# Kernel optimization log

Measured on AMD Instinct MI355X. Metric: run time of the kernel, lower is better.

The kernel has to match this reference:

```python
import jax, jax.numpy as jnp
import numpy as np

N_NODES = 100000


def setup_inputs() -> dict:
    key = jax.random.key(0)
    ks = jax.random.split(key, 6)
    x = jax.random.normal(ks[0], (N_NODES, 128), dtype=jnp.float32)
    edge_index = jax.random.randint(ks[1], (2, 1600000), 0, N_NODES, dtype=jnp.int32)
    W_gcn = jax.random.normal(ks[2], (128, 128), dtype=jnp.float32) * 0.05
    b_gcn = jax.random.normal(ks[3], (128,), dtype=jnp.float32) * 0.05
    W_fc = jax.random.normal(ks[4], (64, 128), dtype=jnp.float32) * 0.05
    b_fc = jax.random.normal(ks[5], (64,), dtype=jnp.float32) * 0.05
    return {"x": x, "edge_index": edge_index, "W_gcn": W_gcn, "b_gcn": b_gcn, "W_fc": W_fc, "b_fc": b_fc}


def _gcn_conv(x, edge_index, W, b):
    N = x.shape[0]
    # add self-loops (PyG GCNConv default add_self_loops=True)
    loops = jnp.arange(N, dtype=edge_index.dtype)
    row = jnp.concatenate([edge_index[0], loops])  # source
    col = jnp.concatenate([edge_index[1], loops])  # target (aggregation index)
    # symmetric normalization: deg computed at target with unit edge weights
    deg = jax.ops.segment_sum(jnp.ones_like(col, dtype=x.dtype), col, num_segments=N)
    deg_inv_sqrt = jnp.where(deg > 0, jax.lax.rsqrt(deg), 0.0)
    norm = deg_inv_sqrt[row] * deg_inv_sqrt[col]  # [E+N]
    xw = x @ W  # [N, nhid] - transform before aggregation
    msgs = norm[:, None] * xw[row]  # gather + scale, [E+N, nhid]
    out = jax.ops.segment_sum(msgs, col, num_segments=N)  # scatter-add
    return out + b


def reference(x, edge_index, W_gcn, b_gcn, W_fc, b_fc):
    h = _gcn_conv(x, edge_index, W_gcn, b_gcn)  # [N, nhid]
    return h @ W_fc.T + b_fc  # [N, nclass]
```

## Files before the change

### kernel.cpp

```cpp
#include <hip/hip_runtime.h>
#include <hip/hip_bf16.h>

typedef __hip_bfloat16 bf16;

#define N_NODES 100000
#define N_EDGES 1600000
#define F_IN    128
#define F_OUT   64
#define NBLK    391

#define NB_BKT   196
#define BKT_SH   9
#define BKT_CAP  8960
#define LBIN_CAP 56
#define EPB_A    4096


typedef __attribute__((ext_vector_type(8))) short vbf8;
typedef __attribute__((ext_vector_type(4))) float vf4;

__device__ __forceinline__ float ldf(const void* p, size_t i, bool isbf) {
    return isbf ? __bfloat162float(((const bf16*)p)[i]) : ((const float*)p)[i];
}
__device__ __forceinline__ void stf(void* p, size_t i, bool isbf, float v) {
    if (isbf) ((bf16*)p)[i] = __float2bfloat16(v);
    else      ((float*)p)[i] = v;
}
__device__ __forceinline__ unsigned short f2bfu(float f) {
    __hip_bfloat16 h = __float2bfloat16(f);
    union { __hip_bfloat16 h; unsigned short u; } c; c.h = h; return c.u;
}
__device__ __forceinline__ float bflo(unsigned int u) { return __uint_as_float(u << 16); }
__device__ __forceinline__ float bfhi(unsigned int u) { return __uint_as_float(u & 0xffff0000u); }

__global__ __launch_bounds__(256) void k_weights(const unsigned short* __restrict__ xs,
                          const void* __restrict__ Wg, const void* __restrict__ bg,
                          const void* __restrict__ Wf, const void* __restrict__ bfc,
                          float* __restrict__ M, float* __restrict__ cvec,
                          bf16* __restrict__ Mhi, bf16* __restrict__ Mlo,
                          int* __restrict__ flag, int* __restrict__ gtail) {
    __shared__ int sflag;
    int lt = threadIdx.x;
    if (lt < 64) {
        int good = 0;
#pragma unroll
        for (int q = 0; q < 2; ++q) {
            unsigned short v = xs[2 * (lt + 64 * q)];
            int e = (v >> 7) & 0xFF;
            if ((e >= 100 && e <= 140) || ((v & 0x7FFF) == 0)) good++;
        }
        unsigned long long m1 = __ballot(good >= 1), m2 = __ballot(good >= 2);
        if (lt == 0) sflag = (__popcll(m1) + __popcll(m2) >= 96) ? 1 : 0;
    }
    __syncthreads();
    bool isbf = (sflag != 0);
    if (blockIdx.x == 0) {
        if (lt == 0) *flag = sflag;
        if (gtail && lt < NB_BKT) gtail[lt] = 0;
    }
    int t = blockIdx.x * 256 + lt;
    if (t >= F_IN * F_OUT) return;
    int k = t >> 6, c = t & 63;
    float s = 0.f;
    for (int j = 0; j < F_IN; ++j)
        s += ldf(Wg, k * F_IN + j, isbf) * ldf(Wf, c * F_IN + j, isbf);
    M[k * F_OUT + c] = s;
    if (Mhi) {
        int l    = (((k >> 3) & 3) << 4) | (c & 15);
        int fidx = ((((k >> 5) << 2) + (c >> 4)) * 64 + l) * 8 + (k & 7);
        bf16 h  = __float2bfloat16(s);
        Mhi[fidx] = h;
        Mlo[fidx] = __float2bfloat16(s - __bfloat162float(h));
    }
    if (k == 0) {
        float cs = ldf(bfc, c, isbf);
        for (int j = 0; j < F_IN; ++j)
            cs += ldf(bg, j, isbf) * ldf(Wf, c * F_IN + j, isbf);
        cvec[c] = cs;
    }
}


__global__ __launch_bounds__(256) void k_binA(const int* __restrict__ ei,
                                              int* __restrict__ gtail,
                                              unsigned* __restrict__ bkt) {
    __shared__ unsigned lbin[NB_BKT * LBIN_CAP];
    __shared__ int lcnt[NB_BKT];
    __shared__ int lbase[NB_BKT];
    int t = threadIdx.x;
    for (int b = t; b < NB_BKT; b += 256) lcnt[b] = 0;
    __syncthreads();
    int v0 = blockIdx.x * (EPB_A / 4);
#pragma unroll
    for (int q = 0; q < 4; ++q) {
        int vi = v0 + q * 256 + t;
        if (vi * 4 < N_EDGES) {
            int4 rv = ((const int4*)ei)[vi];
            int4 cv = ((const int4*)(ei + N_EDGES))[vi];
            int rs[4] = {rv.x, rv.y, rv.z, rv.w};
            int cs[4] = {cv.x, cv.y, cv.z, cv.w};
#pragma unroll
            for (int j = 0; j < 4; ++j) {
                int r = rs[j], c = cs[j];
                int b = c >> BKT_SH;
                unsigned val = (unsigned)r | ((unsigned)(c & ((1 << BKT_SH) - 1)) << 17);
                int p = atomicAdd(&lcnt[b], 1);
                if (p < LBIN_CAP) {
                    lbin[b * LBIN_CAP + p] = val;
                } else {
                    int gp = atomicAdd(&gtail[b], 1);
                    if (gp < BKT_CAP) bkt[(size_t)b * BKT_CAP + gp] = val;
                }
            }
        }
    }
    __syncthreads();
    for (int b = t; b < NB_BKT; b += 256) {
        int n = min(lcnt[b], LBIN_CAP);
        lbase[b] = atomicAdd(&gtail[b], n);
    }
    __syncthreads();
    int w = t >> 6, l = t & 63;
    for (int b = w; b < NB_BKT; b += 4) {
        int nB = min(lcnt[b], LBIN_CAP);
        int gp0 = lbase[b];
        for (int i = l; i < nB; i += 64) {
            int gp = gp0 + i;
            if (gp < BKT_CAP) bkt[(size_t)b * BKT_CAP + gp] = lbin[b * LBIN_CAP + i];
        }
    }
}

__global__ __launch_bounds__(512) void k_build(const unsigned* __restrict__ bkt,
                                               const int* __restrict__ gtail,
                                               int* __restrict__ ptr,
                                               int* __restrict__ cnt,
                                               float* __restrict__ dinv,
                                               int* __restrict__ srcs) {
    __shared__ int cntl[512], sm[512], fill[512];
    int b = blockIdx.x, t = threadIdx.x;
    int n = min(gtail[b], BKT_CAP);
    int gv = (t < b) ? min(gtail[t], BKT_CAP) : 0;
    sm[t] = gv; __syncthreads();
#pragma unroll
    for (int s = 256; s >= 1; s >>= 1) {
        if (t < s) sm[t] += sm[t + s];
        __syncthreads();
    }
    int base = sm[0];
    cntl[t] = 0;
    __syncthreads();
    for (int i = t; i < n; i += 512)
        atomicAdd(&cntl[bkt[(size_t)b * BKT_CAP + i] >> 17], 1);
    __syncthreads();
    int v = cntl[t];
    sm[t] = v; __syncthreads();
    for (int s = 1; s < 512; s <<= 1) {
        int add = (t >= s) ? sm[t - s] : 0;
        __syncthreads();
        sm[t] += add;
        __syncthreads();
    }
    int excl = sm[t] - v;
    fill[t] = excl;
    int node = (b << BKT_SH) + t;
    if (node < N_NODES) {
        ptr[node]  = base + excl;
        cnt[node]  = v;
        dinv[node] = rsqrtf((float)(v + 1));
    }
    __syncthreads();
    for (int i = t; i < n; i += 512) {
        unsigned e = bkt[(size_t)b * BKT_CAP + i];
        int c = (int)(e >> 17);
        int p = atomicAdd(&fill[c], 1);
        srcs[base + p] = (int)(e & 0x1FFFF);
    }
}

__global__ __launch_bounds__(256) void k_xmz_mfma(const int* __restrict__ flag,
                                                  const void* __restrict__ x,
                                                  const bf16* __restrict__ Mhi,
                                                  const bf16* __restrict__ Mlo,
                                                  const float* __restrict__ dinv,
                                                  bf16* __restrict__ y) {
    int t = threadIdx.x;
    int w = t >> 6, lane = t & 63;
    int g = lane >> 4, cb = lane & 15;
    int r0 = blockIdx.x * 64 + w * 16;
    int rr = min(r0 + cb, N_NODES - 1);
    bool isbf = (*flag != 0);
    const vbf8* Bh = (const vbf8*)Mhi;
    const vbf8* Bl = (const vbf8*)Mlo;
    vf4 acc0 = {0.f,0.f,0.f,0.f}, acc1 = {0.f,0.f,0.f,0.f};
    vf4 acc2 = {0.f,0.f,0.f,0.f}, acc3 = {0.f,0.f,0.f,0.f};

    if (isbf) {
        const vbf8* X8 = (const vbf8*)x;
#pragma unroll
        for (int kk = 0; kk < 4; ++kk) {
            vbf8 a = X8[(size_t)rr * 16 + kk * 4 + g];
            int bb = kk * 256 + lane;
            acc0 = __builtin_amdgcn_mfma_f32_16x16x32_bf16(a, Bh[bb      ], acc0, 0, 0, 0);
            acc0 = __builtin_amdgcn_mfma_f32_16x16x32_bf16(a, Bl[bb      ], acc0, 0, 0, 0);
            acc1 = __builtin_amdgcn_mfma_f32_16x16x32_bf16(a, Bh[bb +  64], acc1, 0, 0, 0);
            acc1 = __builtin_amdgcn_mfma_f32_16x16x32_bf16(a, Bl[bb +  64], acc1, 0, 0, 0);
            acc2 = __builtin_amdgcn_mfma_f32_16x16x32_bf16(a, Bh[bb + 128], acc2, 0, 0, 0);
            acc2 = __builtin_amdgcn_mfma_f32_16x16x32_bf16(a, Bl[bb + 128], acc2, 0, 0, 0);
            acc3 = __builtin_amdgcn_mfma_f32_16x16x32_bf16(a, Bh[bb + 192], acc3, 0, 0, 0);
            acc3 = __builtin_amdgcn_mfma_f32_16x16x32_bf16(a, Bl[bb + 192], acc3, 0, 0, 0);
        }
    } else {
        const float4* X4 = (const float4*)x;
#pragma unroll
        for (int kk = 0; kk < 4; ++kk) {
            float4 v0 = X4[(size_t)rr * 32 + kk * 8 + g * 2];
            float4 v1 = X4[(size_t)rr * 32 + kk * 8 + g * 2 + 1];
            vbf8 ah, al;
            {
                float fv[8] = {v0.x, v0.y, v0.z, v0.w, v1.x, v1.y, v1.z, v1.w};
#pragma unroll
                for (int i = 0; i < 8; ++i) {
                    unsigned bi = __float_as_uint(fv[i]);
                    ah[i] = (short)(bi >> 16);
                    float r = fv[i] - __uint_as_float(bi & 0xffff0000u);
                    al[i] = (short)(__float_as_uint(r) >> 16);
                }
            }
            int bb = kk * 256 + lane;
            vbf8 b0h = Bh[bb      ], b0l = Bl[bb      ];
            vbf8 b1h = Bh[bb +  64], b1l = Bl[bb +  64];
            vbf8 b2h = Bh[bb + 128], b2l = Bl[bb + 128];
            vbf8 b3h = Bh[bb + 192], b3l = Bl[bb + 192];
            acc0 = __builtin_amdgcn_mfma_f32_16x16x32_bf16(ah, b0h, acc0, 0, 0, 0);
            acc0 = __builtin_amdgcn_mfma_f32_16x16x32_bf16(ah, b0l, acc0, 0, 0, 0);
            acc0 = __builtin_amdgcn_mfma_f32_16x16x32_bf16(al, b0h, acc0, 0, 0, 0);
            acc1 = __builtin_amdgcn_mfma_f32_16x16x32_bf16(ah, b1h, acc1, 0, 0, 0);
            acc1 = __builtin_amdgcn_mfma_f32_16x16x32_bf16(ah, b1l, acc1, 0, 0, 0);
            acc1 = __builtin_amdgcn_mfma_f32_16x16x32_bf16(al, b1h, acc1, 0, 0, 0);
            acc2 = __builtin_amdgcn_mfma_f32_16x16x32_bf16(ah, b2h, acc2, 0, 0, 0);
            acc2 = __builtin_amdgcn_mfma_f32_16x16x32_bf16(ah, b2l, acc2, 0, 0, 0);
            acc2 = __builtin_amdgcn_mfma_f32_16x16x32_bf16(al, b2h, acc2, 0, 0, 0);
            acc3 = __builtin_amdgcn_mfma_f32_16x16x32_bf16(ah, b3h, acc3, 0, 0, 0);
            acc3 = __builtin_amdgcn_mfma_f32_16x16x32_bf16(ah, b3l, acc3, 0, 0, 0);
            acc3 = __builtin_amdgcn_mfma_f32_16x16x32_bf16(al, b3h, acc3, 0, 0, 0);
        }
    }

    unsigned short* yb = (unsigned short*)y;
#pragma unroll
    for (int i = 0; i < 4; ++i) {
        int r = r0 + g * 4 + i;
        if (r < N_NODES) {
            float d = dinv[r];
            unsigned short* yr = yb + (size_t)r * F_OUT + cb;
            yr[0]  = f2bfu(acc0[i] * d);
            yr[16] = f2bfu(acc1[i] * d);
            yr[32] = f2bfu(acc2[i] * d);
            yr[48] = f2bfu(acc3[i] * d);
        }
    }
}

__global__ __launch_bounds__(256) void k_agg(const int* __restrict__ flag,
                                             const int* __restrict__ ptr,
                                             const int* __restrict__ cnt,
                                             const int* __restrict__ srcs,
                                             const float* __restrict__ dinv,
                                             const bf16* __restrict__ y,
                                             const float* __restrict__ cvec,
                                             void* __restrict__ out) {
    int wid  = (blockIdx.x * 256 + threadIdx.x) >> 6;
    int lane = threadIdx.x & 63;
    int g  = lane >> 3;
    int j8 = lane & 7;
    int node = wid * 8 + g;
    bool alive = node < N_NODES;
    int n = 0, start = 0;
    if (alive) { n = cnt[node]; start = ptr[node]; }
    const uint4* y4 = (const uint4*)y;

    float acc[8];
#pragma unroll
    for (int i = 0; i < 8; ++i) acc[i] = 0.f;

    for (int b = 0; __any(b < n); b += 8) {
        int s = 0;
        int idx = b + j8;
        if (idx < n) s = srcs[start + idx];
#pragma unroll
        for (int k = 0; k < 8; ++k) {
            int su = __shfl(s, (g << 3) | k, 64);
            if (b + k < n) {
                uint4 v = y4[(size_t)su * 8 + j8];
                acc[0] += bflo(v.x); acc[1] += bfhi(v.x);
                acc[2] += bflo(v.y); acc[3] += bfhi(v.y);
                acc[4] += bflo(v.z); acc[5] += bfhi(v.z);
                acc[6] += bflo(v.w); acc[7] += bfhi(v.w);
            }
        }
    }

    if (!alive) return;
    bool isbf = (*flag != 0);
    uint4 sv = y4[(size_t)node * 8 + j8];
    float dn = dinv[node];
    const float4* cv4 = (const float4*)cvec;
    float4 c0 = cv4[j8 * 2], c1 = cv4[j8 * 2 + 1];
    size_t ob = (size_t)node * F_OUT + j8 * 8;
    if (isbf) {
        ushort4 p0, p1;
        p0.x = f2bfu(dn * (acc[0] + bflo(sv.x)) + c0.x);
        p0.y = f2bfu(dn * (acc[1] + bfhi(sv.x)) + c0.y);
        p0.z = f2bfu(dn * (acc[2] + bflo(sv.y)) + c0.z);
        p0.w = f2bfu(dn * (acc[3] + bfhi(sv.y)) + c0.w);
        p1.x = f2bfu(dn * (acc[4] + bflo(sv.z)) + c1.x);
        p1.y = f2bfu(dn * (acc[5] + bfhi(sv.z)) + c1.y);
        p1.z = f2bfu(dn * (acc[6] + bflo(sv.w)) + c1.z);
        p1.w = f2bfu(dn * (acc[7] + bfhi(sv.w)) + c1.w);
        ushort4* ob4 = (ushort4*)((unsigned short*)out + ob);
        ob4[0] = p0; ob4[1] = p1;
    } else {
        float4 q0, q1;
        q0.x = dn * (acc[0] + bflo(sv.x)) + c0.x;
        q0.y = dn * (acc[1] + bfhi(sv.x)) + c0.y;
        q0.z = dn * (acc[2] + bflo(sv.y)) + c0.z;
        q0.w = dn * (acc[3] + bfhi(sv.y)) + c0.w;
        q1.x = dn * (acc[4] + bflo(sv.z)) + c1.x;
        q1.y = dn * (acc[5] + bfhi(sv.z)) + c1.y;
        q1.z = dn * (acc[6] + bflo(sv.w)) + c1.z;
        q1.w = dn * (acc[7] + bfhi(sv.w)) + c1.w;
        float4* of4 = (float4*)((float*)out + ob);
        of4[0] = q0; of4[1] = q1;
    }
}


__global__ void k_init_deg(float* __restrict__ deg) {
    int i = blockIdx.x * blockDim.x + threadIdx.x;
    if (i < N_NODES) deg[i] = 1.0f;
}
__global__ void k_deg(const int* __restrict__ col, float* __restrict__ deg) {
    int e = blockIdx.x * blockDim.x + threadIdx.x;
    if (e < N_EDGES) atomicAdd(&deg[col[e]], 1.0f);
}
__global__ void k_dinv(float* __restrict__ deg) {
    int i = blockIdx.x * blockDim.x + threadIdx.x;
    if (i < N_NODES) deg[i] = rsqrtf(deg[i]);
}
__global__ __launch_bounds__(256) void k_xm(const int* __restrict__ flag,
                                            const void* __restrict__ x,
                                            const float* __restrict__ M,
                                            void* __restrict__ z) {
    __shared__ float Ms[F_IN * F_OUT];
    int t = threadIdx.x;
    for (int i = t; i < F_IN * F_OUT; i += 256) Ms[i] = M[i];
    __syncthreads();
    bool isbf = (*flag != 0);
    int r = blockIdx.x * 4 + (t >> 6);
    int c = t & 63;
    if (r >= N_NODES) return;
    float s = 0.f;
    if (isbf) {
        const bf16* xr = (const bf16*)x + (size_t)r * F_IN;
#pragma unroll
        for (int k = 0; k < F_IN; ++k) s += __bfloat162float(xr[k]) * Ms[k * F_OUT + c];
    } else {
        const float* xr = (const float*)x + (size_t)r * F_IN;
#pragma unroll
        for (int k = 0; k < F_IN; ++k) s += xr[k] * Ms[k * F_OUT + c];
    }
    stf(z, (size_t)r * F_OUT + c, isbf, s);
}
template <int LOGF>
__global__ __launch_bounds__(256) void k_init_acc(const int* __restrict__ flag,
                                                  const float* __restrict__ dinv,
                                                  const void* __restrict__ z,
                                                  float* __restrict__ acc, int base) {
    bool isbf = (*flag != 0);
    int t = blockIdx.x * 256 + threadIdx.x;
    int i = t >> LOGF, f = t & ((1 << LOGF) - 1);
    if (i >= N_NODES) return;
    float d = dinv[i];
    acc[t] = d * d * ldf(z, (size_t)i * F_OUT + base + f, isbf);
}
template <int LOGF>
__global__ __launch_bounds__(256) void k_scatter(const int* __restrict__ flag,
                                                 const int* __restrict__ ei,
                                                 const float* __restrict__ dinv,
                                                 const void* __restrict__ z,
                                                 float* __restrict__ acc, int base) {
    bool isbf = (*flag != 0);
    long long t = (long long)blockIdx.x * 256 + threadIdx.x;
    int e = (int)(t >> LOGF), f = (int)(t & ((1 << LOGF) - 1));
    if (e >= N_EDGES) return;
    int r = ei[e], c = ei[N_EDGES + e];
    float nm = dinv[r] * dinv[c];
    float v  = nm * ldf(z, (size_t)r * F_OUT + base + f, isbf);
    atomicAdd(&acc[((size_t)c << LOGF) + f], v);
}
template <int LOGF>
__global__ __launch_bounds__(256) void k_final(const int* __restrict__ flag,
                                               const float* __restrict__ acc,
                                               const float* __restrict__ cvec,
                                               void* __restrict__ out, int base) {
    bool isbf = (*flag != 0);
    int t = blockIdx.x * 256 + threadIdx.x;
    int i = t >> LOGF, f = t & ((1 << LOGF) - 1);
    if (i >= N_NODES) return;
    stf(out, (size_t)i * F_OUT + base + f, isbf, acc[t] + cvec[base + f]);
}
template <int LOGF>
static void run_passes(const int* flag, const int* ei, const float* dinv,
                       const void* z, float* acc, const float* cvec, void* out,
                       hipStream_t stream) {
    const int fpp = 1 << LOGF;
    const long long tn = (long long)N_NODES * fpp;
    const long long te = (long long)N_EDGES * fpp;
    const int gn = (int)((tn + 255) / 256);
    const int ge = (int)((te + 255) / 256);
    for (int base = 0; base < F_OUT; base += fpp) {
        k_init_acc<LOGF><<<gn, 256, 0, stream>>>(flag, dinv, z, acc, base);
        k_scatter<LOGF><<<ge, 256, 0, stream>>>(flag, ei, dinv, z, acc, base);
        k_final<LOGF><<<gn, 256, 0, stream>>>(flag, acc, cvec, out, base);
    }
}

extern "C" void kernel_launch(void* const* d_in, const int* in_sizes, int n_in,
                              void* d_out, int out_size, void* d_ws, size_t ws_size,
                              hipStream_t stream) {
    const void* x   = d_in[0];
    const int*  ei  = (const int*)d_in[1];
    const void* Wg  = d_in[2];
    const void* bg  = d_in[3];
    const void* Wf  = d_in[4];
    const void* bfc = d_in[5];
    char* ws = (char*)d_ws;

    const size_t CSR_NEED = 20871168;
    if (ws_size >= CSR_NEED) {
        int*      flag  = (int*)(ws + 0);
        float*    dinv  = (float*)(ws + 256);
        float*    M     = (float*)(ws + 400384);
        float*    cvec  = (float*)(ws + 433152);
        int*      cnt   = (int*)(ws + 433664);
        int*      ptr   = (int*)(ws + 833664);
        int*      gtail = (int*)(ws + 1233664);
        int*      srcs  = (int*)(ws + 1238528);
        bf16*     y     = (bf16*)(ws + 8038400);
        unsigned* bkt   = (unsigned*)(ws + 8038400);
        bf16*     Mhi   = (bf16*)(ws + 20838400);
        bf16*     Mlo   = (bf16*)(ws + 20854784);

        k_weights<<<(F_IN * F_OUT) / 256, 256, 0, stream>>>((const unsigned short*)x,
                    Wg, bg, Wf, bfc, M, cvec, Mhi, Mlo, flag, gtail);
        k_binA<<<(N_EDGES + EPB_A - 1) / EPB_A, 256, 0, stream>>>(ei, gtail, bkt);
        k_build<<<NB_BKT, 512, 0, stream>>>(bkt, gtail, ptr, cnt, dinv, srcs);
        k_xmz_mfma<<<(N_NODES + 63) / 64, 256, 0, stream>>>(flag, x, Mhi, Mlo, dinv, y);
        k_agg<<<3125, 256, 0, stream>>>(flag, ptr, cnt, srcs, dinv, y, cvec, d_out);
    } else {
        int*   flag = (int*)(ws + 0);
        float* deg  = (float*)(ws + 256);
        float* M    = (float*)(ws + 400384);
        float* cvec = (float*)(ws + 433152);
        float* acc  = (float*)(ws + 433664);

        k_weights<<<(F_IN * F_OUT) / 256, 256, 0, stream>>>((const unsigned short*)x,
                    Wg, bg, Wf, bfc, M, cvec, (bf16*)nullptr, (bf16*)nullptr, flag, (int*)nullptr);
        k_init_deg<<<NBLK, 256, 0, stream>>>(deg);
        k_deg<<<N_EDGES / 256, 256, 0, stream>>>(ei + N_EDGES, deg);
        k_dinv<<<NBLK, 256, 0, stream>>>(deg);
        k_xm<<<N_NODES / 4, 256, 0, stream>>>(flag, x, M, d_out);
        const size_t bn = 433664;
        if      (ws_size >= bn + (400000ull << 6)) run_passes<6>(flag, ei, deg, d_out, acc, cvec, d_out, stream);
        else if (ws_size >= bn + (400000ull << 5)) run_passes<5>(flag, ei, deg, d_out, acc, cvec, d_out, stream);
        else if (ws_size >= bn + (400000ull << 4)) run_passes<4>(flag, ei, deg, d_out, acc, cvec, d_out, stream);
        else if (ws_size >= bn + (400000ull << 3)) run_passes<3>(flag, ei, deg, d_out, acc, cvec, d_out, stream);
        else if (ws_size >= bn + (400000ull << 2)) run_passes<2>(flag, ei, deg, d_out, acc, cvec, d_out, stream);
        else if (ws_size >= bn + (400000ull << 1)) run_passes<1>(flag, ei, deg, d_out, acc, cvec, d_out, stream);
        else                                       run_passes<0>(flag, ei, deg, d_out, acc, cvec, d_out, stream);
    }
}
```

Baseline: 214.9 us.

## Replace bucketed CSR build with atomic degree count, block-scan pointers, atomic scatter

The CSR construction no longer uses two-level bucketing through shared-memory bins. It now counts in-degrees with global atomics fused into the weights kernel, computes row pointers with per-block scans whose bases come from an atomic tail counter, and scatters source indices through per-node cursor atomics. This removes the bucket staging buffer and a pass over the edges, at the cost of many scattered global atomics and non-deterministic ordering of sources within each row. Row segments are also placed in atomic-arrival order rather than node order.

```diff
diff --git a/kernel.cpp b/kernel.cpp
--- a/kernel.cpp
+++ b/kernel.cpp
@@ -9,12 +9,6 @@
 #define F_OUT   64
 #define NBLK    391
 
-#define NB_BKT   196
-#define BKT_SH   9
-#define BKT_CAP  8960
-#define LBIN_CAP 56
-#define EPB_A    4096
-
 
 typedef __attribute__((ext_vector_type(8))) short vbf8;
 typedef __attribute__((ext_vector_type(4))) float vf4;
@@ -38,7 +32,8 @@
                           const void* __restrict__ Wf, const void* __restrict__ bfc,
                           float* __restrict__ M, float* __restrict__ cvec,
                           bf16* __restrict__ Mhi, bf16* __restrict__ Mlo,
-                          int* __restrict__ flag, int* __restrict__ gtail) {
+                          int* __restrict__ flag, int* __restrict__ tail,
+                          int* __restrict__ deg, const int* __restrict__ col) {
     __shared__ int sflag;
     int lt = threadIdx.x;
     if (lt < 64) {
@@ -54,9 +49,17 @@
     }
     __syncthreads();
     bool isbf = (sflag != 0);
-    if (blockIdx.x == 0) {
-        if (lt == 0) *flag = sflag;
-        if (gtail && lt < NB_BKT) gtail[lt] = 0;
+    if (blockIdx.x == 0 && lt == 0) {
+        *flag = sflag;
+        if (tail) *tail = 0;
+    }
+    if (deg) {
+        const int4* c4 = (const int4*)col;
+        for (int vi = blockIdx.x * 256 + lt; vi < N_EDGES / 4; vi += gridDim.x * 256) {
+            int4 cv = c4[vi];
+            atomicAdd(&deg[cv.x], 1); atomicAdd(&deg[cv.y], 1);
+            atomicAdd(&deg[cv.z], 1); atomicAdd(&deg[cv.w], 1);
+        }
     }
     int t = blockIdx.x * 256 + lt;
     if (t >= F_IN * F_OUT) return;
@@ -81,101 +84,45 @@
 }
 
 
-__global__ __launch_bounds__(256) void k_binA(const int* __restrict__ ei,
-                                              int* __restrict__ gtail,
-                                              unsigned* __restrict__ bkt) {
-    __shared__ unsigned lbin[NB_BKT * LBIN_CAP];
-    __shared__ int lcnt[NB_BKT];
-    __shared__ int lbase[NB_BKT];
+__global__ __launch_bounds__(256) void k_ptr(const int* __restrict__ deg,
+                                             int* __restrict__ tail,
+                                             int* __restrict__ ptr,
+                                             int* __restrict__ cursor,
+                                             float* __restrict__ dinv) {
+    __shared__ int sm[256];
+    __shared__ int sbase;
     int t = threadIdx.x;
-    for (int b = t; b < NB_BKT; b += 256) lcnt[b] = 0;
-    __syncthreads();
-    int v0 = blockIdx.x * (EPB_A / 4);
-#pragma unroll
-    for (int q = 0; q < 4; ++q) {
-        int vi = v0 + q * 256 + t;
-        if (vi * 4 < N_EDGES) {
-            int4 rv = ((const int4*)ei)[vi];
-            int4 cv = ((const int4*)(ei + N_EDGES))[vi];
-            int rs[4] = {rv.x, rv.y, rv.z, rv.w};
-            int cs[4] = {cv.x, cv.y, cv.z, cv.w};
-#pragma unroll
-            for (int j = 0; j < 4; ++j) {
-                int r = rs[j], c = cs[j];
-                int b = c >> BKT_SH;
-                unsigned val = (unsigned)r | ((unsigned)(c & ((1 << BKT_SH) - 1)) << 17);
-                int p = atomicAdd(&lcnt[b], 1);
-                if (p < LBIN_CAP) {
-                    lbin[b * LBIN_CAP + p] = val;
-                } else {
-                    int gp = atomicAdd(&gtail[b], 1);
-                    if (gp < BKT_CAP) bkt[(size_t)b * BKT_CAP + gp] = val;
-                }
-            }
-        }
-    }
-    __syncthreads();
-    for (int b = t; b < NB_BKT; b += 256) {
-        int n = min(lcnt[b], LBIN_CAP);
-        lbase[b] = atomicAdd(&gtail[b], n);
-    }
-    __syncthreads();
-    int w = t >> 6, l = t & 63;
-    for (int b = w; b < NB_BKT; b += 4) {
-        int nB = min(lcnt[b], LBIN_CAP);
-        int gp0 = lbase[b];
-        for (int i = l; i < nB; i += 64) {
-            int gp = gp0 + i;
-            if (gp < BKT_CAP) bkt[(size_t)b * BKT_CAP + gp] = lbin[b * LBIN_CAP + i];
-        }
-    }
-}
-
-__global__ __launch_bounds__(512) void k_build(const unsigned* __restrict__ bkt,
-                                               const int* __restrict__ gtail,
-                                               int* __restrict__ ptr,
-                                               int* __restrict__ cnt,
-                                               float* __restrict__ dinv,
-                                               int* __restrict__ srcs) {
-    __shared__ int cntl[512], sm[512], fill[512];
-    int b = blockIdx.x, t = threadIdx.x;
-    int n = min(gtail[b], BKT_CAP);
-    int gv = (t < b) ? min(gtail[t], BKT_CAP) : 0;
-    sm[t] = gv; __syncthreads();
-#pragma unroll
-    for (int s = 256; s >= 1; s >>= 1) {
-        if (t < s) sm[t] += sm[t + s];
-        __syncthreads();
-    }
-    int base = sm[0];
-    cntl[t] = 0;
-    __syncthreads();
-    for (int i = t; i < n; i += 512)
-        atomicAdd(&cntl[bkt[(size_t)b * BKT_CAP + i] >> 17], 1);
-    __syncthreads();
-    int v = cntl[t];
+    int node = blockIdx.x * 256 + t;
+    int v = (node < N_NODES) ? deg[node] : 0;
     sm[t] = v; __syncthreads();
-    for (int s = 1; s < 512; s <<= 1) {
+    for (int s = 1; s < 256; s <<= 1) {
         int add = (t >= s) ? sm[t - s] : 0;
         __syncthreads();
         sm[t] += add;
         __syncthreads();
     }
-    int excl = sm[t] - v;
-    fill[t] = excl;
-    int node = (b << BKT_SH) + t;
+    if (t == 255) sbase = atomicAdd(tail, sm[255]);
+    __syncthreads();
     if (node < N_NODES) {
-        ptr[node]  = base + excl;
-        cnt[node]  = v;
-        dinv[node] = rsqrtf((float)(v + 1));
-    }
-    __syncthreads();
-    for (int i = t; i < n; i += 512) {
-        unsigned e = bkt[(size_t)b * BKT_CAP + i];
-        int c = (int)(e >> 17);
-        int p = atomicAdd(&fill[c], 1);
-        srcs[base + p] = (int)(e & 0x1FFFF);
-    }
+        int p = sbase + sm[t] - v;
+        ptr[node]    = p;
+        cursor[node] = p;
+        dinv[node]   = rsqrtf((float)(v + 1));
+    }
+}
+
+__global__ __launch_bounds__(256) void k_scat(const int* __restrict__ ei,
+                                              int* __restrict__ cursor,
+                                              int* __restrict__ srcs) {
+    int vi = blockIdx.x * 256 + threadIdx.x;
+    if (vi >= N_EDGES / 4) return;
+    int4 rv = ((const int4*)ei)[vi];
+    int4 cv = ((const int4*)(ei + N_EDGES))[vi];
+    int p;
+    p = atomicAdd(&cursor[cv.x], 1); srcs[p] = rv.x;
+    p = atomicAdd(&cursor[cv.y], 1); srcs[p] = rv.y;
+    p = atomicAdd(&cursor[cv.z], 1); srcs[p] = rv.z;
+    p = atomicAdd(&cursor[cv.w], 1); srcs[p] = rv.w;
 }
 
 __global__ __launch_bounds__(256) void k_xmz_mfma(const int* __restrict__ flag,
@@ -439,25 +386,27 @@
 
     const size_t CSR_NEED = 20871168;
     if (ws_size >= CSR_NEED) {
-        int*      flag  = (int*)(ws + 0);
-        float*    dinv  = (float*)(ws + 256);
-        float*    M     = (float*)(ws + 400384);
-        float*    cvec  = (float*)(ws + 433152);
-        int*      cnt   = (int*)(ws + 433664);
-        int*      ptr   = (int*)(ws + 833664);
-        int*      gtail = (int*)(ws + 1233664);
-        int*      srcs  = (int*)(ws + 1238528);
-        bf16*     y     = (bf16*)(ws + 8038400);
-        unsigned* bkt   = (unsigned*)(ws + 8038400);
-        bf16*     Mhi   = (bf16*)(ws + 20838400);
-        bf16*     Mlo   = (bf16*)(ws + 20854784);
-
-        k_weights<<<(F_IN * F_OUT) / 256, 256, 0, stream>>>((const unsigned short*)x,
-                    Wg, bg, Wf, bfc, M, cvec, Mhi, Mlo, flag, gtail);
-        k_binA<<<(N_EDGES + EPB_A - 1) / EPB_A, 256, 0, stream>>>(ei, gtail, bkt);
-        k_build<<<NB_BKT, 512, 0, stream>>>(bkt, gtail, ptr, cnt, dinv, srcs);
+        int*      flag   = (int*)(ws + 0);
+        float*    dinv   = (float*)(ws + 256);
+        int*      tail   = (int*)(ws + 400256);
+        float*    M      = (float*)(ws + 400384);
+        float*    cvec   = (float*)(ws + 433152);
+        int*      deg    = (int*)(ws + 433664);
+        int*      ptr    = (int*)(ws + 833664);
+        int*      srcs   = (int*)(ws + 1238528);
+        bf16*     y      = (bf16*)(ws + 8038400);
+        int*      cursor = (int*)(ws + 8038400);
+        bf16*     Mhi    = (bf16*)(ws + 20838400);
+        bf16*     Mlo    = (bf16*)(ws + 20854784);
+
+        hipMemsetAsync(deg, 0, (size_t)N_NODES * 4, stream);
+        k_weights<<<512, 256, 0, stream>>>((const unsigned short*)x,
+                    Wg, bg, Wf, bfc, M, cvec, Mhi, Mlo, flag, tail,
+                    deg, ei + N_EDGES);
+        k_ptr<<<NBLK, 256, 0, stream>>>(deg, tail, ptr, cursor, dinv);
+        k_scat<<<(N_EDGES / 4 + 255) / 256, 256, 0, stream>>>(ei, cursor, srcs);
         k_xmz_mfma<<<(N_NODES + 63) / 64, 256, 0, stream>>>(flag, x, Mhi, Mlo, dinv, y);
-        k_agg<<<3125, 256, 0, stream>>>(flag, ptr, cnt, srcs, dinv, y, cvec, d_out);
+        k_agg<<<3125, 256, 0, stream>>>(flag, ptr, deg, srcs, dinv, y, cvec, d_out);
     } else {
         int*   flag = (int*)(ws + 0);
         float* deg  = (float*)(ws + 256);
@@ -466,7 +415,8 @@
         float* acc  = (float*)(ws + 433664);
 
         k_weights<<<(F_IN * F_OUT) / 256, 256, 0, stream>>>((const unsigned short*)x,
-                    Wg, bg, Wf, bfc, M, cvec, (bf16*)nullptr, (bf16*)nullptr, flag, (int*)nullptr);
+                    Wg, bg, Wf, bfc, M, cvec, (bf16*)nullptr, (bf16*)nullptr,
+                    flag, (int*)nullptr, (int*)nullptr, (const int*)nullptr);
         k_init_deg<<<NBLK, 256, 0, stream>>>(deg);
         k_deg<<<N_EDGES / 256, 256, 0, stream>>>(ei + N_EDGES, deg);
         k_dinv<<<NBLK, 256, 0, stream>>>(deg);
```

New measurement: 372.1 us. +73.2%, slower.

## Fuse weight prep with edge binning, and CSR build with feature transform

Applied to the files above, without the earlier changes.

The weight-precompute and edge-binning kernels become one launch, split by block index. CSR build and the MFMA feature transform also become one launch, so they run side by side instead of in sequence. To remove the transform's dependence on the build's dinv, the binning pass also counts in-degree with global atomics, and the transform computes its own normalization from that count. The bucket buffer is moved so it no longer aliases y, and two memsets zero the counters. This trades launch gaps and serialization for 1.6M extra random global atomics and two extra memset launches.

```diff
diff --git a/kernel.cpp b/kernel.cpp
--- a/kernel.cpp
+++ b/kernel.cpp
@@ -14,6 +14,8 @@
 #define BKT_CAP  8960
 #define LBIN_CAP 56
 #define EPB_A    4096
+#define WBLK     32
+#define XMZ_BLK  782
 
 
 typedef __attribute__((ext_vector_type(8))) short vbf8;
@@ -33,64 +35,61 @@
 __device__ __forceinline__ float bflo(unsigned int u) { return __uint_as_float(u << 16); }
 __device__ __forceinline__ float bfhi(unsigned int u) { return __uint_as_float(u & 0xffff0000u); }
 
-__global__ __launch_bounds__(256) void k_weights(const unsigned short* __restrict__ xs,
+__global__ __launch_bounds__(256) void k_fat1(const unsigned short* __restrict__ xs,
                           const void* __restrict__ Wg, const void* __restrict__ bg,
                           const void* __restrict__ Wf, const void* __restrict__ bfc,
                           float* __restrict__ M, float* __restrict__ cvec,
                           bf16* __restrict__ Mhi, bf16* __restrict__ Mlo,
-                          int* __restrict__ flag, int* __restrict__ gtail) {
-    __shared__ int sflag;
-    int lt = threadIdx.x;
-    if (lt < 64) {
-        int good = 0;
-#pragma unroll
-        for (int q = 0; q < 2; ++q) {
-            unsigned short v = xs[2 * (lt + 64 * q)];
-            int e = (v >> 7) & 0xFF;
-            if ((e >= 100 && e <= 140) || ((v & 0x7FFF) == 0)) good++;
-        }
-        unsigned long long m1 = __ballot(good >= 1), m2 = __ballot(good >= 2);
-        if (lt == 0) sflag = (__popcll(m1) + __popcll(m2) >= 96) ? 1 : 0;
-    }
-    __syncthreads();
-    bool isbf = (sflag != 0);
-    if (blockIdx.x == 0) {
-        if (lt == 0) *flag = sflag;
-        if (gtail && lt < NB_BKT) gtail[lt] = 0;
-    }
-    int t = blockIdx.x * 256 + lt;
-    if (t >= F_IN * F_OUT) return;
-    int k = t >> 6, c = t & 63;
-    float s = 0.f;
-    for (int j = 0; j < F_IN; ++j)
-        s += ldf(Wg, k * F_IN + j, isbf) * ldf(Wf, c * F_IN + j, isbf);
-    M[k * F_OUT + c] = s;
-    if (Mhi) {
-        int l    = (((k >> 3) & 3) << 4) | (c & 15);
-        int fidx = ((((k >> 5) << 2) + (c >> 4)) * 64 + l) * 8 + (k & 7);
-        bf16 h  = __float2bfloat16(s);
-        Mhi[fidx] = h;
-        Mlo[fidx] = __float2bfloat16(s - __bfloat162float(h));
-    }
-    if (k == 0) {
-        float cs = ldf(bfc, c, isbf);
-        for (int j = 0; j < F_IN; ++j)
-            cs += ldf(bg, j, isbf) * ldf(Wf, c * F_IN + j, isbf);
-        cvec[c] = cs;
-    }
-}
-
-
-__global__ __launch_bounds__(256) void k_binA(const int* __restrict__ ei,
-                                              int* __restrict__ gtail,
-                                              unsigned* __restrict__ bkt) {
+                          int* __restrict__ flag,
+                          const int* __restrict__ ei, int* __restrict__ gtail,
+                          unsigned* __restrict__ bkt, int* __restrict__ deg) {
     __shared__ unsigned lbin[NB_BKT * LBIN_CAP];
     __shared__ int lcnt[NB_BKT];
     __shared__ int lbase[NB_BKT];
-    int t = threadIdx.x;
+    __shared__ int sflag;
+    int lt = threadIdx.x;
+
+    if (blockIdx.x < WBLK) {
+        if (lt < 64) {
+            int good = 0;
+#pragma unroll
+            for (int q = 0; q < 2; ++q) {
+                unsigned short v = xs[2 * (lt + 64 * q)];
+                int e = (v >> 7) & 0xFF;
+                if ((e >= 100 && e <= 140) || ((v & 0x7FFF) == 0)) good++;
+            }
+            unsigned long long m1 = __ballot(good >= 1), m2 = __ballot(good >= 2);
+            if (lt == 0) sflag = (__popcll(m1) + __popcll(m2) >= 96) ? 1 : 0;
+        }
+        __syncthreads();
+        bool isbf = (sflag != 0);
+        if (blockIdx.x == 0 && lt == 0) *flag = sflag;
+        int t = blockIdx.x * 256 + lt;
+        int k = t >> 6, c = t & 63;
+        float s = 0.f;
+        for (int j = 0; j < F_IN; ++j)
+            s += ldf(Wg, k * F_IN + j, isbf) * ldf(Wf, c * F_IN + j, isbf);
+        M[k * F_OUT + c] = s;
+        if (Mhi) {
+            int l    = (((k >> 3) & 3) << 4) | (c & 15);
+            int fidx = ((((k >> 5) << 2) + (c >> 4)) * 64 + l) * 8 + (k & 7);
+            bf16 h  = __float2bfloat16(s);
+            Mhi[fidx] = h;
+            Mlo[fidx] = __float2bfloat16(s - __bfloat162float(h));
+        }
+        if (k == 0) {
+            float cs = ldf(bfc, c, isbf);
+            for (int j = 0; j < F_IN; ++j)
+                cs += ldf(bg, j, isbf) * ldf(Wf, c * F_IN + j, isbf);
+            cvec[c] = cs;
+        }
+        return;
+    }
+
+    int t = lt;
     for (int b = t; b < NB_BKT; b += 256) lcnt[b] = 0;
     __syncthreads();
-    int v0 = blockIdx.x * (EPB_A / 4);
+    int v0 = (blockIdx.x - WBLK) * (EPB_A / 4);
 #pragma unroll
     for (int q = 0; q < 4; ++q) {
         int vi = v0 + q * 256 + t;
@@ -102,6 +101,7 @@
 #pragma unroll
             for (int j = 0; j < 4; ++j) {
                 int r = rs[j], c = cs[j];
+                atomicAdd(&deg[c], 1);
                 int b = c >> BKT_SH;
                 unsigned val = (unsigned)r | ((unsigned)(c & ((1 << BKT_SH) - 1)) << 17);
                 int p = atomicAdd(&lcnt[b], 1);
@@ -131,63 +131,67 @@
     }
 }
 
-__global__ __launch_bounds__(512) void k_build(const unsigned* __restrict__ bkt,
-                                               const int* __restrict__ gtail,
-                                               int* __restrict__ ptr,
-                                               int* __restrict__ cnt,
-                                               float* __restrict__ dinv,
-                                               int* __restrict__ srcs) {
+__global__ __launch_bounds__(512) void k_fat2(const unsigned* __restrict__ bkt,
+                                              const int* __restrict__ gtail,
+                                              int* __restrict__ ptr,
+                                              int* __restrict__ cnt,
+                                              float* __restrict__ dinv,
+                                              int* __restrict__ srcs,
+                                              const int* __restrict__ flag,
+                                              const void* __restrict__ x,
+                                              const bf16* __restrict__ Mhi,
+                                              const bf16* __restrict__ Mlo,
+                                              const int* __restrict__ deg,
+                                              bf16* __restrict__ y) {
     __shared__ int cntl[512], sm[512], fill[512];
-    int b = blockIdx.x, t = threadIdx.x;
-    int n = min(gtail[b], BKT_CAP);
-    int gv = (t < b) ? min(gtail[t], BKT_CAP) : 0;
-    sm[t] = gv; __syncthreads();
-#pragma unroll
-    for (int s = 256; s >= 1; s >>= 1) {
-        if (t < s) sm[t] += sm[t + s];
+    int t = threadIdx.x;
+
+    if (blockIdx.x < NB_BKT) {
+        int b = blockIdx.x;
+        int n = min(gtail[b], BKT_CAP);
+        int gv = (t < b) ? min(gtail[t], BKT_CAP) : 0;
+        sm[t] = gv; __syncthreads();
+#pragma unroll
+        for (int s = 256; s >= 1; s >>= 1) {
+            if (t < s) sm[t] += sm[t + s];
+            __syncthreads();
+        }
+        int base = sm[0];
+        cntl[t] = 0;
         __syncthreads();
-    }
-    int base = sm[0];
-    cntl[t] = 0;
-    __syncthreads();
-    for (int i = t; i < n; i += 512)
-        atomicAdd(&cntl[bkt[(size_t)b * BKT_CAP + i] >> 17], 1);
-    __syncthreads();
-    int v = cntl[t];
-    sm[t] = v; __syncthreads();
-    for (int s = 1; s < 512; s <<= 1) {
-        int add = (t >= s) ? sm[t - s] : 0;
+        for (int i = t; i < n; i += 512)
+            atomicAdd(&cntl[bkt[(size_t)b * BKT_CAP + i] >> 17], 1);
         __syncthreads();
-        sm[t] += add;
+        int v = cntl[t];
+        sm[t] = v; __syncthreads();
+        for (int s = 1; s < 512; s <<= 1) {
+            int add = (t >= s) ? sm[t - s] : 0;
+            __syncthreads();
+            sm[t] += add;
+            __syncthreads();
+        }
+        int excl = sm[t] - v;
+        fill[t] = excl;
+        int node = (b << BKT_SH) + t;
+        if (node < N_NODES) {
+            ptr[node]  = base + excl;
+            cnt[node]  = v;
+            dinv[node] = rsqrtf((float)(v + 1));
+        }
         __syncthreads();
-    }
-    int excl = sm[t] - v;
-    fill[t] = excl;
-    int node = (b << BKT_SH) + t;
-    if (node < N_NODES) {
-        ptr[node]  = base + excl;
-        cnt[node]  = v;
-        dinv[node] = rsqrtf((float)(v + 1));
-    }
-    __syncthreads();
-    for (int i = t; i < n; i += 512) {
-        unsigned e = bkt[(size_t)b * BKT_CAP + i];
-        int c = (int)(e >> 17);
-        int p = atomicAdd(&fill[c], 1);
-        srcs[base + p] = (int)(e & 0x1FFFF);
-    }
-}
-
-__global__ __launch_bounds__(256) void k_xmz_mfma(const int* __restrict__ flag,
-                                                  const void* __restrict__ x,
-                                                  const bf16* __restrict__ Mhi,
-                                                  const bf16* __restrict__ Mlo,
-                                                  const float* __restrict__ dinv,
-                                                  bf16* __restrict__ y) {
-    int t = threadIdx.x;
+        for (int i = t; i < n; i += 512) {
+            unsigned e = bkt[(size_t)b * BKT_CAP + i];
+            int c = (int)(e >> 17);
+            int p = atomicAdd(&fill[c], 1);
+            srcs[base + p] = (int)(e & 0x1FFFF);
+        }
+        return;
+    }
+
+    int bid = blockIdx.x - NB_BKT;
     int w = t >> 6, lane = t & 63;
     int g = lane >> 4, cb = lane & 15;
-    int r0 = blockIdx.x * 64 + w * 16;
+    int r0 = bid * 128 + w * 16;
     int rr = min(r0 + cb, N_NODES - 1);
     bool isbf = (*flag != 0);
     const vbf8* Bh = (const vbf8*)Mhi;
@@ -252,7 +256,7 @@
     for (int i = 0; i < 4; ++i) {
         int r = r0 + g * 4 + i;
         if (r < N_NODES) {
-            float d = dinv[r];
+            float d = rsqrtf((float)(deg[r] + 1));
             unsigned short* yr = yb + (size_t)r * F_OUT + cb;
             yr[0]  = f2bfu(acc0[i] * d);
             yr[16] = f2bfu(acc1[i] * d);
@@ -437,7 +441,7 @@
     const void* bfc = d_in[5];
     char* ws = (char*)d_ws;
 
-    const size_t CSR_NEED = 20871168;
+    const size_t CSR_NEED = 28295808;
     if (ws_size >= CSR_NEED) {
         int*      flag  = (int*)(ws + 0);
         float*    dinv  = (float*)(ws + 256);
@@ -448,15 +452,18 @@
         int*      gtail = (int*)(ws + 1233664);
         int*      srcs  = (int*)(ws + 1238528);
         bf16*     y     = (bf16*)(ws + 8038400);
-        unsigned* bkt   = (unsigned*)(ws + 8038400);
         bf16*     Mhi   = (bf16*)(ws + 20838400);
         bf16*     Mlo   = (bf16*)(ws + 20854784);
-
-        k_weights<<<(F_IN * F_OUT) / 256, 256, 0, stream>>>((const unsigned short*)x,
-                    Wg, bg, Wf, bfc, M, cvec, Mhi, Mlo, flag, gtail);
-        k_binA<<<(N_EDGES + EPB_A - 1) / EPB_A, 256, 0, stream>>>(ei, gtail, bkt);
-        k_build<<<NB_BKT, 512, 0, stream>>>(bkt, gtail, ptr, cnt, dinv, srcs);
-        k_xmz_mfma<<<(N_NODES + 63) / 64, 256, 0, stream>>>(flag, x, Mhi, Mlo, dinv, y);
+        unsigned* bkt   = (unsigned*)(ws + 20871168);
+        int*      deg   = (int*)(ws + 27895808);
+
+        hipMemsetAsync(gtail, 0, NB_BKT * 4, stream);
+        hipMemsetAsync(deg, 0, (size_t)N_NODES * 4, stream);
+        k_fat1<<<WBLK + (N_EDGES + EPB_A - 1) / EPB_A, 256, 0, stream>>>(
+                    (const unsigned short*)x, Wg, bg, Wf, bfc, M, cvec, Mhi, Mlo,
+                    flag, ei, gtail, bkt, deg);
+        k_fat2<<<NB_BKT + XMZ_BLK, 512, 0, stream>>>(bkt, gtail, ptr, cnt, dinv,
+                    srcs, flag, x, Mhi, Mlo, deg, y);
         k_agg<<<3125, 256, 0, stream>>>(flag, ptr, cnt, srcs, dinv, y, cvec, d_out);
     } else {
         int*   flag = (int*)(ws + 0);
@@ -465,8 +472,10 @@
         float* cvec = (float*)(ws + 433152);
         float* acc  = (float*)(ws + 433664);
 
-        k_weights<<<(F_IN * F_OUT) / 256, 256, 0, stream>>>((const unsigned short*)x,
-                    Wg, bg, Wf, bfc, M, cvec, (bf16*)nullptr, (bf16*)nullptr, flag, (int*)nullptr);
+        k_fat1<<<WBLK, 256, 0, stream>>>((const unsigned short*)x,
+                    Wg, bg, Wf, bfc, M, cvec, (bf16*)nullptr, (bf16*)nullptr,
+                    flag, (const int*)nullptr, (int*)nullptr,
+                    (unsigned*)nullptr, (int*)nullptr);
         k_init_deg<<<NBLK, 256, 0, stream>>>(deg);
         k_deg<<<N_EDGES / 256, 256, 0, stream>>>(ei + N_EDGES, deg);
         k_dinv<<<NBLK, 256, 0, stream>>>(deg);
```

Result: slower. 238.9 us (+11.2%).

## Fuse CSR build with MFMA transform by deferring source normalization to aggregation

Applied to the files above, without the earlier changes.

The CSR build and the x·M MFMA transform now run in one launch as heterogeneous blocks. This works because the transform no longer scales rows by dinv. The source-side normalization moves into the aggregation loop, which multiplies each gathered row by dinv[src]. The bucket buffer gets its own workspace region instead of aliasing the transform output, which raises the workspace requirement. This removes a launch and a serialization point, at the cost of an extra per-edge dinv gather and multiplies in aggregation.

```diff
diff --git a/kernel.cpp b/kernel.cpp
--- a/kernel.cpp
+++ b/kernel.cpp
@@ -14,6 +14,7 @@
 #define BKT_CAP  8960
 #define LBIN_CAP 56
 #define EPB_A    4096
+#define XMZ_BLK  782
 
 
 typedef __attribute__((ext_vector_type(8))) short vbf8;
@@ -131,63 +132,66 @@
     }
 }
 
-__global__ __launch_bounds__(512) void k_build(const unsigned* __restrict__ bkt,
-                                               const int* __restrict__ gtail,
-                                               int* __restrict__ ptr,
-                                               int* __restrict__ cnt,
-                                               float* __restrict__ dinv,
-                                               int* __restrict__ srcs) {
+__global__ __launch_bounds__(512) void k_fat2(const unsigned* __restrict__ bkt,
+                                              const int* __restrict__ gtail,
+                                              int* __restrict__ ptr,
+                                              int* __restrict__ cnt,
+                                              float* __restrict__ dinv,
+                                              int* __restrict__ srcs,
+                                              const int* __restrict__ flag,
+                                              const void* __restrict__ x,
+                                              const bf16* __restrict__ Mhi,
+                                              const bf16* __restrict__ Mlo,
+                                              bf16* __restrict__ z) {
     __shared__ int cntl[512], sm[512], fill[512];
-    int b = blockIdx.x, t = threadIdx.x;
-    int n = min(gtail[b], BKT_CAP);
-    int gv = (t < b) ? min(gtail[t], BKT_CAP) : 0;
-    sm[t] = gv; __syncthreads();
-#pragma unroll
-    for (int s = 256; s >= 1; s >>= 1) {
-        if (t < s) sm[t] += sm[t + s];
+    int t = threadIdx.x;
+
+    if (blockIdx.x < NB_BKT) {
+        int b = blockIdx.x;
+        int n = min(gtail[b], BKT_CAP);
+        int gv = (t < b) ? min(gtail[t], BKT_CAP) : 0;
+        sm[t] = gv; __syncthreads();
+#pragma unroll
+        for (int s = 256; s >= 1; s >>= 1) {
+            if (t < s) sm[t] += sm[t + s];
+            __syncthreads();
+        }
+        int base = sm[0];
+        cntl[t] = 0;
         __syncthreads();
-    }
-    int base = sm[0];
-    cntl[t] = 0;
-    __syncthreads();
-    for (int i = t; i < n; i += 512)
-        atomicAdd(&cntl[bkt[(size_t)b * BKT_CAP + i] >> 17], 1);
-    __syncthreads();
-    int v = cntl[t];
-    sm[t] = v; __syncthreads();
-    for (int s = 1; s < 512; s <<= 1) {
-        int add = (t >= s) ? sm[t - s] : 0;
+        for (int i = t; i < n; i += 512)
+            atomicAdd(&cntl[bkt[(size_t)b * BKT_CAP + i] >> 17], 1);
         __syncthreads();
-        sm[t] += add;
+        int v = cntl[t];
+        sm[t] = v; __syncthreads();
+        for (int s = 1; s < 512; s <<= 1) {
+            int add = (t >= s) ? sm[t - s] : 0;
+            __syncthreads();
+            sm[t] += add;
+            __syncthreads();
+        }
+        int excl = sm[t] - v;
+        fill[t] = excl;
+        int node = (b << BKT_SH) + t;
+        if (node < N_NODES) {
+            ptr[node]  = base + excl;
+            cnt[node]  = v;
+            dinv[node] = rsqrtf((float)(v + 1));
+        }
         __syncthreads();
-    }
-    int excl = sm[t] - v;
-    fill[t] = excl;
-    int node = (b << BKT_SH) + t;
-    if (node < N_NODES) {
-        ptr[node]  = base + excl;
-        cnt[node]  = v;
-        dinv[node] = rsqrtf((float)(v + 1));
-    }
-    __syncthreads();
-    for (int i = t; i < n; i += 512) {
-        unsigned e = bkt[(size_t)b * BKT_CAP + i];
-        int c = (int)(e >> 17);
-        int p = atomicAdd(&fill[c], 1);
-        srcs[base + p] = (int)(e & 0x1FFFF);
-    }
-}
-
-__global__ __launch_bounds__(256) void k_xmz_mfma(const int* __restrict__ flag,
-                                                  const void* __restrict__ x,
-                                                  const bf16* __restrict__ Mhi,
-                                                  const bf16* __restrict__ Mlo,
-                                                  const float* __restrict__ dinv,
-                                                  bf16* __restrict__ y) {
-    int t = threadIdx.x;
+        for (int i = t; i < n; i += 512) {
+            unsigned e = bkt[(size_t)b * BKT_CAP + i];
+            int c = (int)(e >> 17);
+            int p = atomicAdd(&fill[c], 1);
+            srcs[base + p] = (int)(e & 0x1FFFF);
+        }
+        return;
+    }
+
+    int bid = blockIdx.x - NB_BKT;
     int w = t >> 6, lane = t & 63;
     int g = lane >> 4, cb = lane & 15;
-    int r0 = blockIdx.x * 64 + w * 16;
+    int r0 = bid * 128 + w * 16;
     int rr = min(r0 + cb, N_NODES - 1);
     bool isbf = (*flag != 0);
     const vbf8* Bh = (const vbf8*)Mhi;
@@ -247,17 +251,16 @@
         }
     }
 
-    unsigned short* yb = (unsigned short*)y;
+    unsigned short* zb = (unsigned short*)z;
 #pragma unroll
     for (int i = 0; i < 4; ++i) {
         int r = r0 + g * 4 + i;
         if (r < N_NODES) {
-            float d = dinv[r];
-            unsigned short* yr = yb + (size_t)r * F_OUT + cb;
-            yr[0]  = f2bfu(acc0[i] * d);
-            yr[16] = f2bfu(acc1[i] * d);
-            yr[32] = f2bfu(acc2[i] * d);
-            yr[48] = f2bfu(acc3[i] * d);
+            unsigned short* zr = zb + (size_t)r * F_OUT + cb;
+            zr[0]  = f2bfu(acc0[i]);
+            zr[16] = f2bfu(acc1[i]);
+            zr[32] = f2bfu(acc2[i]);
+            zr[48] = f2bfu(acc3[i]);
         }
     }
 }
@@ -267,7 +270,7 @@
                                              const int* __restrict__ cnt,
                                              const int* __restrict__ srcs,
                                              const float* __restrict__ dinv,
-                                             const bf16* __restrict__ y,
+                                             const bf16* __restrict__ z,
                                              const float* __restrict__ cvec,
                                              void* __restrict__ out) {
     int wid  = (blockIdx.x * 256 + threadIdx.x) >> 6;
@@ -278,7 +281,7 @@
     bool alive = node < N_NODES;
     int n = 0, start = 0;
     if (alive) { n = cnt[node]; start = ptr[node]; }
-    const uint4* y4 = (const uint4*)y;
+    const uint4* z4 = (const uint4*)z;
 
     float acc[8];
 #pragma unroll
@@ -292,44 +295,45 @@
         for (int k = 0; k < 8; ++k) {
             int su = __shfl(s, (g << 3) | k, 64);
             if (b + k < n) {
-                uint4 v = y4[(size_t)su * 8 + j8];
-                acc[0] += bflo(v.x); acc[1] += bfhi(v.x);
-                acc[2] += bflo(v.y); acc[3] += bfhi(v.y);
-                acc[4] += bflo(v.z); acc[5] += bfhi(v.z);
-                acc[6] += bflo(v.w); acc[7] += bfhi(v.w);
+                float ds = dinv[su];
+                uint4 v = z4[(size_t)su * 8 + j8];
+                acc[0] += ds * bflo(v.x); acc[1] += ds * bfhi(v.x);
+                acc[2] += ds * bflo(v.y); acc[3] += ds * bfhi(v.y);
+                acc[4] += ds * bflo(v.z); acc[5] += ds * bfhi(v.z);
+                acc[6] += ds * bflo(v.w); acc[7] += ds * bfhi(v.w);
             }
         }
     }
 
     if (!alive) return;
     bool isbf = (*flag != 0);
-    uint4 sv = y4[(size_t)node * 8 + j8];
+    uint4 sv = z4[(size_t)node * 8 + j8];
     float dn = dinv[node];
     const float4* cv4 = (const float4*)cvec;
     float4 c0 = cv4[j8 * 2], c1 = cv4[j8 * 2 + 1];
     size_t ob = (size_t)node * F_OUT + j8 * 8;
     if (isbf) {
         ushort4 p0, p1;
-        p0.x = f2bfu(dn * (acc[0] + bflo(sv.x)) + c0.x);
-        p0.y = f2bfu(dn * (acc[1] + bfhi(sv.x)) + c0.y);
-        p0.z = f2bfu(dn * (acc[2] + bflo(sv.y)) + c0.z);
-        p0.w = f2bfu(dn * (acc[3] + bfhi(sv.y)) + c0.w);
-        p1.x = f2bfu(dn * (acc[4] + bflo(sv.z)) + c1.x);
-        p1.y = f2bfu(dn * (acc[5] + bfhi(sv.z)) + c1.y);
-        p1.z = f2bfu(dn * (acc[6] + bflo(sv.w)) + c1.z);
-        p1.w = f2bfu(dn * (acc[7] + bfhi(sv.w)) + c1.w);
+        p0.x = f2bfu(dn * (acc[0] + dn * bflo(sv.x)) + c0.x);
+        p0.y = f2bfu(dn * (acc[1] + dn * bfhi(sv.x)) + c0.y);
+        p0.z = f2bfu(dn * (acc[2] + dn * bflo(sv.y)) + c0.z);
+        p0.w = f2bfu(dn * (acc[3] + dn * bfhi(sv.y)) + c0.w);
+        p1.x = f2bfu(dn * (acc[4] + dn * bflo(sv.z)) + c1.x);
+        p1.y = f2bfu(dn * (acc[5] + dn * bfhi(sv.z)) + c1.y);
+        p1.z = f2bfu(dn * (acc[6] + dn * bflo(sv.w)) + c1.z);
+        p1.w = f2bfu(dn * (acc[7] + dn * bfhi(sv.w)) + c1.w);
         ushort4* ob4 = (ushort4*)((unsigned short*)out + ob);
         ob4[0] = p0; ob4[1] = p1;
     } else {
         float4 q0, q1;
-        q0.x = dn * (acc[0] + bflo(sv.x)) + c0.x;
-        q0.y = dn * (acc[1] + bfhi(sv.x)) + c0.y;
-        q0.z = dn * (acc[2] + bflo(sv.y)) + c0.z;
-        q0.w = dn * (acc[3] + bfhi(sv.y)) + c0.w;
-        q1.x = dn * (acc[4] + bflo(sv.z)) + c1.x;
-        q1.y = dn * (acc[5] + bfhi(sv.z)) + c1.y;
-        q1.z = dn * (acc[6] + bflo(sv.w)) + c1.z;
-        q1.w = dn * (acc[7] + bfhi(sv.w)) + c1.w;
+        q0.x = dn * (acc[0] + dn * bflo(sv.x)) + c0.x;
+        q0.y = dn * (acc[1] + dn * bfhi(sv.x)) + c0.y;
+        q0.z = dn * (acc[2] + dn * bflo(sv.y)) + c0.z;
+        q0.w = dn * (acc[3] + dn * bfhi(sv.y)) + c0.w;
+        q1.x = dn * (acc[4] + dn * bflo(sv.z)) + c1.x;
+        q1.y = dn * (acc[5] + dn * bfhi(sv.z)) + c1.y;
+        q1.z = dn * (acc[6] + dn * bflo(sv.w)) + c1.z;
+        q1.w = dn * (acc[7] + dn * bfhi(sv.w)) + c1.w;
         float4* of4 = (float4*)((float*)out + ob);
         of4[0] = q0; of4[1] = q1;
     }
@@ -437,7 +441,7 @@
     const void* bfc = d_in[5];
     char* ws = (char*)d_ws;
 
-    const size_t CSR_NEED = 20871168;
+    const size_t CSR_NEED = 27895808;
     if (ws_size >= CSR_NEED) {
         int*      flag  = (int*)(ws + 0);
         float*    dinv  = (float*)(ws + 256);
@@ -447,17 +451,17 @@
         int*      ptr   = (int*)(ws + 833664);
         int*      gtail = (int*)(ws + 1233664);
         int*      srcs  = (int*)(ws + 1238528);
-        bf16*     y     = (bf16*)(ws + 8038400);
-        unsigned* bkt   = (unsigned*)(ws + 8038400);
+        bf16*     z     = (bf16*)(ws + 8038400);
         bf16*     Mhi   = (bf16*)(ws + 20838400);
         bf16*     Mlo   = (bf16*)(ws + 20854784);
+        unsigned* bkt   = (unsigned*)(ws + 20871168);
 
         k_weights<<<(F_IN * F_OUT) / 256, 256, 0, stream>>>((const unsigned short*)x,
                     Wg, bg, Wf, bfc, M, cvec, Mhi, Mlo, flag, gtail);
         k_binA<<<(N_EDGES + EPB_A - 1) / EPB_A, 256, 0, stream>>>(ei, gtail, bkt);
-        k_build<<<NB_BKT, 512, 0, stream>>>(bkt, gtail, ptr, cnt, dinv, srcs);
-        k_xmz_mfma<<<(N_NODES + 63) / 64, 256, 0, stream>>>(flag, x, Mhi, Mlo, dinv, y);
-        k_agg<<<3125, 256, 0, stream>>>(flag, ptr, cnt, srcs, dinv, y, cvec, d_out);
+        k_fat2<<<NB_BKT + XMZ_BLK, 512, 0, stream>>>(bkt, gtail, ptr, cnt, dinv,
+                    srcs, flag, x, Mhi, Mlo, z);
+        k_agg<<<3125, 256, 0, stream>>>(flag, ptr, cnt, srcs, dinv, z, cvec, d_out);
     } else {
         int*   flag = (int*)(ws + 0);
         float* deg  = (float*)(ws + 256);
```

Measured after the change: 204.8 us. -4.7%, faster.
